# Kernel optimization log

Hardware: AMD Instinct MI355X
Metric: run time of the kernel (lower is better)

## Reference

```python
import jax, jax.numpy as jnp
from jax import lax
import numpy as np

EPS = 4e-3            # geoopt float32 ball boundary eps
MAXNORM = 1.0 - EPS   # c = 1 Poincare ball


def _norm(x):
    return jnp.sqrt(jnp.maximum(jnp.sum(x * x, axis=-1, keepdims=True), 1e-15))


def expmap0(u):
    n = _norm(u)
    return jnp.tanh(n) * u / n


def projx(x):
    n = _norm(x)
    return jnp.where(n > MAXNORM, x * (MAXNORM / n), x)


def mobius_add(x, y):
    x2 = jnp.sum(x * x, -1, keepdims=True)
    y2 = jnp.sum(y * y, -1, keepdims=True)
    xy = jnp.sum(x * y, -1, keepdims=True)
    num = (1.0 + 2.0 * xy + y2) * x + (1.0 - x2) * y
    den = 1.0 + 2.0 * xy + x2 * y2
    return num / jnp.maximum(den, 1e-15)


def mamba_layer(x, inW, convW, convb, xpW, dtW, dtb, A_log, Dp, outW):
    # x: [B,T,H]; inW: [2*Din,H]; convW: [Din,K]; xpW: [R+2N,Din]; dtW: [Din,R]
    B, T, H = x.shape
    Din, N = A_log.shape
    K = convW.shape[-1]
    R = dtW.shape[-1]
    xz = jnp.einsum('bth,dh->btd', x, inW)              # [B,T,2*Din]
    xr, z = jnp.split(xz, 2, axis=-1)
    xc = lax.conv_general_dilated(jnp.transpose(xr, (0, 2, 1)), convW[:, None, :],
                                  (1,), [(K - 1, 0)], feature_group_count=Din)
    u = jax.nn.silu(jnp.transpose(xc + convb[None, :, None], (0, 2, 1)))  # [B,T,Din]
    x_dbl = jnp.einsum('btd,ed->bte', u, xpW)           # [B,T,R+2N]
    dt_r, Bm, Cm = x_dbl[..., :R], x_dbl[..., R:R + N], x_dbl[..., R + N:]
    dt = jax.nn.softplus(jnp.einsum('btr,dr->btd', dt_r, dtW) + dtb)      # [B,T,Din]
    A = -jnp.exp(A_log)                                 # [Din,N]
    dA = jnp.exp(dt[..., None] * A)                     # [B,T,Din,N]
    dBu = dt[..., None] * Bm[:, :, None, :] * u[..., None]

    def step(h, ins):
        dA_t, dBu_t, C_t = ins
        h = dA_t * h + dBu_t                            # [B,Din,N]
        return h, jnp.einsum('bdn,bn->bd', h, C_t)

    h0 = jnp.zeros((B, Din, N), x.dtype)
    _, ys = lax.scan(step, h0, (jnp.moveaxis(dA, 1, 0), jnp.moveaxis(dBu, 1, 0), jnp.moveaxis(Cm, 1, 0)))
    y = jnp.moveaxis(ys, 0, 1) + Dp * u                 # [B,T,Din]
    return jnp.einsum('btd,hd->bth', y * jax.nn.silu(z), outW)


def _encode(xs, inp_W, inp_b, in_proj_W, conv_W, conv_b, xproj_W, dt_W, dt_b, A_log, D_skip, out_W, outp_W, outp_b):
    # xs: [4,B,T,1]; params carry leading branch dim 4, then layer dim 3
    def branch(x, iW, ib, ipW, cW, cb, xpW, dW, db, Al, Dp, oW, opW, opb):
        h = jnp.einsum('bti,hi->bth', x, iW) + ib
        for l in range(ipW.shape[0]):
            h = mamba_layer(h, ipW[l], cW[l], cb[l], xpW[l], dW[l], db[l], Al[l], Dp[l], oW[l])
        return jnp.tanh(jnp.einsum('bth,eh->bte', h, opW) + opb)
    return jax.vmap(branch)(xs, inp_W, inp_b, in_proj_W, conv_W, conv_b, xproj_W, dt_W, dt_b, A_log, D_skip, out_W, outp_W, outp_b)


def setup_inputs() -> dict:
    key = jax.random.key(0)
    ks = jax.random.split(key, 24)
    Br, B, T, H, Din, N, K, R, E, L = 4, 32, 1024, 64, 128, 16, 4, 4, 32, 3

    def rn(k, shape, s=0.05):
        return jax.random.normal(k, shape, jnp.float32) * s

    A_init = jnp.log(jnp.arange(1, N + 1, dtype=jnp.float32))
    return {
        'trend': jax.random.normal(ks[0], (B, T, 1), jnp.float32),
        'seasonal_weekly': jax.random.normal(ks[1], (B, T, 1), jnp.float32),
        'seasonal_daily': jax.random.normal(ks[2], (B, T, 1), jnp.float32),
        'residual': jax.random.normal(ks[3], (B, T, 1), jnp.float32),
        'inp_W': rn(ks[4], (Br, H, 1), 0.5),
        'inp_b': rn(ks[5], (Br, H)),
        'in_proj_W': rn(ks[6], (Br, L, 2 * Din, H)),
        'conv_W': rn(ks[7], (Br, L, Din, K), 0.2),
        'conv_b': rn(ks[8], (Br, L, Din)),
        'xproj_W': rn(ks[9], (Br, L, R + 2 * N, Din)),
        'dt_W': rn(ks[10], (Br, L, Din, R), 0.2),
        'dt_b': rn(ks[11], (Br, L, Din), 0.5) - 4.0,  # softplus(dt_b) small
        'A_log': jnp.tile(A_init, (Br, L, Din, 1)) + rn(ks[12], (Br, L, Din, N), 0.01),
        'D_skip': jnp.ones((Br, L, Din), jnp.float32) + rn(ks[13], (Br, L, Din), 0.01),
        'out_W': rn(ks[14], (Br, L, H, Din)),
        'outp_W': rn(ks[15], (Br, E, H)),
        'outp_b': rn(ks[16], (Br, E)),
    }


def reference(trend, seasonal_weekly, seasonal_daily, residual, inp_W, inp_b, in_proj_W, conv_W, conv_b, xproj_W, dt_W, dt_b, A_log, D_skip, out_W, outp_W, outp_b):
    xs = jnp.stack([trend, seasonal_weekly, seasonal_daily, residual], 0)  # [4,B,T,1]
    z = _encode(xs, inp_W, inp_b, in_proj_W, conv_W, conv_b, xproj_W, dt_W, dt_b, A_log, D_skip, out_W, outp_W, outp_b)  # [4,B,T,E]
    zh = projx(expmap0(z))
    t, w, d, r = zh[0], zh[1], zh[2], zh[3]
    comb = projx(mobius_add(mobius_add(t, mobius_add(w, d)), r))
    # stacked [trend_h, weekly_h, daily_h, residual_h, combined_h]
    return jnp.stack([t, w, d, r, comb], 0)
```

## Files before the change

kernel.cpp:

```cpp
#include <hip/hip_runtime.h>
#include <math.h>

#define TT 1024
#define DIN 128
#define HH 64
#define NN 16
#define EE 32
#define LL 3
#define BB 32

__device__ __forceinline__ float siluf(float x) { return x / (1.f + __expf(-x)); }

typedef __attribute__((ext_vector_type(8))) short bf16x8;
typedef __attribute__((ext_vector_type(4))) float f32x4;

__device__ __forceinline__ void split2(float x, ushort& hi, ushort& lo) {
  unsigned u = __float_as_uint(x);
  hi = (ushort)(u >> 16);
  float rem = x - __uint_as_float((u >> 16) << 16);
  lo = (ushort)(__float_as_uint(rem) >> 16);
}

__global__ __launch_bounds__(256) void k_xz(
    const float* __restrict__ x0, const float* __restrict__ x1,
    const float* __restrict__ x2, const float* __restrict__ x3,
    const float* __restrict__ h, const float* __restrict__ inprojW,
    const float* __restrict__ inpW, const float* __restrict__ inpb,
    float* __restrict__ xr, float* __restrict__ zb, int br0, int l) {
  __shared__ __align__(16) ushort Hh[64][72], Hl[64][72];
  __shared__ __align__(16) ushort Wh[64][72], Wl[64][72];
  const int tid = threadIdx.x;
  const int b  = blockIdx.y;
  const int t0 = blockIdx.x * 64;
  const int br = br0 + (b >> 5);
  const float* Hg = h + ((size_t)b * TT + t0) * HH;
  const int row = tid >> 2, c0 = (tid & 3) * 16;
  {
    float xv = 0.f;
    if (l == 0) {
      int bb = b & 31;
      const float* xp = (br == 0) ? x0 : (br == 1) ? x1 : (br == 2) ? x2 : x3;
      xv = xp[bb * TT + t0 + row];
    }
    #pragma unroll
    for (int q = 0; q < 4; ++q) {
      float4 hv;
      if (l == 0) {
        float4 w4 = *(const float4*)(inpW + br * HH + c0 + q * 4);
        float4 b4 = *(const float4*)(inpb + br * HH + c0 + q * 4);
        hv.x = xv * w4.x + b4.x; hv.y = xv * w4.y + b4.y;
        hv.z = xv * w4.z + b4.z; hv.w = xv * w4.w + b4.w;
      } else {
        hv = *(const float4*)(Hg + (size_t)row * HH + c0 + q * 4);
      }
      ushort h0,h1,h2,h3,l0,l1,l2,l3;
      split2(hv.x,h0,l0); split2(hv.y,h1,l1); split2(hv.z,h2,l2); split2(hv.w,h3,l3);
      *(ushort4*)&Hh[row][c0 + q*4] = make_ushort4(h0,h1,h2,h3);
      *(ushort4*)&Hl[row][c0 + q*4] = make_ushort4(l0,l1,l2,l3);
    }
  }
  const int wave = tid >> 6, lane = tid & 63;
  const int quad = lane >> 4, l16 = lane & 15;
  const int nsub = (wave & 1) * 32, tsub = (wave >> 1) * 32;
  for (int n0 = 0; n0 < 2 * DIN; n0 += 64) {
    const float* Wg = inprojW + (size_t)((br * LL + l) * 2 * DIN + n0) * HH;
    {
      #pragma unroll
      for (int q = 0; q < 4; ++q) {
        float4 wv = *(const float4*)(Wg + (size_t)row * HH + c0 + q * 4);
        ushort h0,h1,h2,h3,l0,l1,l2,l3;
        split2(wv.x,h0,l0); split2(wv.y,h1,l1); split2(wv.z,h2,l2); split2(wv.w,h3,l3);
        *(ushort4*)&Wh[row][c0 + q*4] = make_ushort4(h0,h1,h2,h3);
        *(ushort4*)&Wl[row][c0 + q*4] = make_ushort4(l0,l1,l2,l3);
      }
    }
    __syncthreads();
    f32x4 acc[2][2] = {};
    #pragma unroll
    for (int k0 = 0; k0 < 64; k0 += 32) {
      bf16x8 Ah[2], Al[2], Bh[2], Bl[2];
      #pragma unroll
      for (int i = 0; i < 2; ++i) {
        Ah[i] = *(const bf16x8*)&Wh[nsub + i*16 + l16][k0 + quad*8];
        Al[i] = *(const bf16x8*)&Wl[nsub + i*16 + l16][k0 + quad*8];
        Bh[i] = *(const bf16x8*)&Hh[tsub + i*16 + l16][k0 + quad*8];
        Bl[i] = *(const bf16x8*)&Hl[tsub + i*16 + l16][k0 + quad*8];
      }
      #pragma unroll
      for (int i = 0; i < 2; ++i)
        #pragma unroll
        for (int j = 0; j < 2; ++j) {
          acc[i][j] = __builtin_amdgcn_mfma_f32_16x16x32_bf16(Ah[i], Bh[j], acc[i][j], 0, 0, 0);
          acc[i][j] = __builtin_amdgcn_mfma_f32_16x16x32_bf16(Ah[i], Bl[j], acc[i][j], 0, 0, 0);
          acc[i][j] = __builtin_amdgcn_mfma_f32_16x16x32_bf16(Al[i], Bh[j], acc[i][j], 0, 0, 0);
        }
    }
    #pragma unroll
    for (int i = 0; i < 2; ++i) {
      #pragma unroll
      for (int r = 0; r < 4; ++r) {
        int n = n0 + nsub + i*16 + quad*4 + r;
        float* dst = (n < DIN) ? (xr + ((size_t)b * DIN + n) * TT)
                               : (zb + ((size_t)b * DIN + (n - DIN)) * TT);
        #pragma unroll
        for (int j = 0; j < 2; ++j)
          dst[t0 + tsub + j*16 + l16] = acc[i][j][r];
      }
    }
    __syncthreads();
  }
}

__global__ __launch_bounds__(256) void k_xdbl(
    const float* __restrict__ xr, const float* __restrict__ convW,
    const float* __restrict__ convb, const float* __restrict__ xprojW,
    const float* __restrict__ dtW, const float* __restrict__ dtb,
    float* __restrict__ u, float* __restrict__ dt,
    float* __restrict__ Bm, float* __restrict__ Cm,
    int br0, int l) {
  __shared__ __align__(16) float Xr[16][72];
  __shared__ __align__(16) float As2[32][68];
  __shared__ __align__(16) float Ws2[32][48];
  __shared__ __align__(16) float Xs[40][68];
  const int tid = threadIdx.x;
  const int b  = blockIdx.y;
  const int t0 = blockIdx.x * 64;
  const int br = br0 + (b >> 5);
  const float* W = xprojW + (size_t)((br * LL + l) * 36) * DIN;
  const int rowk = tid >> 4, c4 = tid & 15;
  const int wave = tid >> 6, lane = tid & 63;
  const int quad = lane >> 4, l16 = lane & 15;
  const int tw = wave * 16;
  f32x4 acc[3] = {};
  for (int k0 = 0; k0 < DIN; k0 += 32) {
    #pragma unroll
    for (int ks = 0; ks < 32; ks += 16) {
      __syncthreads();
      {
        const float* src = xr + ((size_t)b * DIN + k0 + ks + rowk) * TT + t0;
        *(float4*)&Xr[rowk][4 + c4 * 4] = *(const float4*)(src + c4 * 4);
        if (tid < 16) {
          float4 hv = make_float4(0.f, 0.f, 0.f, 0.f);
          if (t0 > 0) hv = *(const float4*)(xr + ((size_t)b * DIN + k0 + ks + tid) * TT + t0 - 4);
          *(float4*)&Xr[tid][0] = hv;
        }
      }
      __syncthreads();
      {
        int d = k0 + ks + rowk;
        const float* w = convW + (size_t)((br * LL + l) * DIN + d) * 4;
        float w0 = w[0], w1 = w[1], w2 = w[2], w3 = w[3];
        float cb = convb[(br * LL + l) * DIN + d];
        int i0 = c4 * 4;
        float o[4];
        #pragma unroll
        for (int q = 0; q < 4; ++q) {
          int j = i0 + q;
          float a = Xr[rowk][j+1]*w0 + Xr[rowk][j+2]*w1 + Xr[rowk][j+3]*w2 + Xr[rowk][j+4]*w3 + cb;
          o[q] = siluf(a);
        }
        float4 uo = make_float4(o[0], o[1], o[2], o[3]);
        *(float4*)&As2[ks + rowk][i0] = uo;
        *(float4*)(u + ((size_t)b * DIN + d) * TT + t0 + i0) = uo;
      }
    }
    for (int idx = tid; idx < 1536; idx += 256) {
      int jj = idx >> 5, kk = idx & 31;
      Ws2[kk][jj] = (jj < 36) ? W[(size_t)jj * DIN + k0 + kk] : 0.f;
    }
    __syncthreads();
    ushort bh[8], bl[8];
    #pragma unroll
    for (int j = 0; j < 8; ++j) {
      float v = As2[quad * 8 + j][tw + l16];
      split2(v, bh[j], bl[j]);
    }
    bf16x8 Bh = *(bf16x8*)bh, Bl = *(bf16x8*)bl;
    #pragma unroll
    for (int nf = 0; nf < 3; ++nf) {
      ushort wh[8], wl[8];
      #pragma unroll
      for (int j = 0; j < 8; ++j) {
        float v = Ws2[quad * 8 + j][nf * 16 + l16];
        split2(v, wh[j], wl[j]);
      }
      bf16x8 Wh = *(bf16x8*)wh, Wl = *(bf16x8*)wl;
      acc[nf] = __builtin_amdgcn_mfma_f32_16x16x32_bf16(Wh, Bh, acc[nf], 0, 0, 0);
      acc[nf] = __builtin_amdgcn_mfma_f32_16x16x32_bf16(Wh, Bl, acc[nf], 0, 0, 0);
      acc[nf] = __builtin_amdgcn_mfma_f32_16x16x32_bf16(Wl, Bh, acc[nf], 0, 0, 0);
    }
  }
  __syncthreads();
  #pragma unroll
  for (int nf = 0; nf < 3; ++nf) {
    #pragma unroll
    for (int r = 0; r < 4; ++r) {
      int n = nf * 16 + quad * 4 + r;
      if (n < 40) Xs[n][tw + l16] = acc[nf][r];
    }
  }
  __syncthreads();
  {
    int n = tid >> 4, i0 = (tid & 15) * 4;
    *(float4*)(Bm + ((size_t)b * NN + n) * TT + t0 + i0) = *(float4*)&Xs[4 + n][i0];
    *(float4*)(Cm + ((size_t)b * NN + n) * TT + t0 + i0) = *(float4*)&Xs[20 + n][i0];
  }
  {
    int d = tid >> 1, half = tid & 1;
    const float* wd = dtW + (size_t)((br * LL + l) * DIN + d) * 4;
    float w0 = wd[0], w1 = wd[1], w2 = wd[2], w3 = wd[3];
    float bias = dtb[(br * LL + l) * DIN + d];
    float* dtp = dt + ((size_t)b * DIN + d) * TT + t0 + half * 32;
    #pragma unroll
    for (int g8 = 0; g8 < 8; ++g8) {
      float o[4];
      #pragma unroll
      for (int q = 0; q < 4; ++q) {
        int i = half * 32 + g8 * 4 + q;
        float s = Xs[0][i]*w0 + Xs[1][i]*w1 + Xs[2][i]*w2 + Xs[3][i]*w3 + bias;
        float e = __expf(-fabsf(s));
        o[q] = fmaxf(s, 0.f) + __logf(1.f + e);
      }
      *(float4*)(dtp + g8*4) = make_float4(o[0], o[1], o[2], o[3]);
    }
  }
}

__global__ __launch_bounds__(256) void k_scan1(
    const float* __restrict__ dtc, const float* __restrict__ u,
    const float* __restrict__ Bm, const float* __restrict__ Cm,
    const float* __restrict__ A_log, const float* __restrict__ D_skip,
    float* __restrict__ Hloc, float* __restrict__ g, float* __restrict__ sdt,
    int br0, int l) {
  __shared__ __align__(16) float Bl[16][66];
  __shared__ __align__(16) float Cl[16][66];
  const int bx  = blockIdx.x;
  const int b   = bx >> 5;
  const int rem = bx & 31;
  const int c   = rem >> 1;
  const int dh  = rem & 1;
  const int tid = threadIdx.x;
  {
    int row = tid >> 4, cc = (tid & 15) * 4;
    float4 bv = *(const float4*)(Bm + ((size_t)b * NN + row) * TT + c * 64 + cc);
    *(float2*)&Bl[row][cc]     = make_float2(bv.x, bv.y);
    *(float2*)&Bl[row][cc + 2] = make_float2(bv.z, bv.w);
    float4 cv = *(const float4*)(Cm + ((size_t)b * NN + row) * TT + c * 64 + cc);
    *(float2*)&Cl[row][cc]     = make_float2(cv.x, cv.y);
    *(float2*)&Cl[row][cc + 2] = make_float2(cv.z, cv.w);
  }
  __syncthreads();
  const int d  = dh * 64 + (tid >> 2);
  const int n0 = (tid & 3) * 4;
  const int br = br0 + (b >> 5);
  const int wbase = (br * LL + l) * DIN + d;
  float Ac[4];
  #pragma unroll
  for (int j = 0; j < 4; ++j) Ac[j] = -__expf(A_log[(size_t)wbase * NN + n0 + j]);
  float Dp = D_skip[wbase];
  const float* dtp = dtc + ((size_t)b * DIN + d) * TT + c * 64;
  const float* up = u + ((size_t)b * DIN + d) * TT + c * 64;
  float* gp = g + ((size_t)b * DIN + d) * TT + c * 64;
  float hst[4] = {0.f, 0.f, 0.f, 0.f};
  float sd = 0.f;
  for (int t0 = 0; t0 < 64; t0 += 8) {
    float4 dq0 = *(const float4*)(dtp + t0);
    float4 dq1 = *(const float4*)(dtp + t0 + 4);
    float4 uq0 = *(const float4*)(up + t0);
    float4 uq1 = *(const float4*)(up + t0 + 4);
    float dts[8] = {dq0.x, dq0.y, dq0.z, dq0.w, dq1.x, dq1.y, dq1.z, dq1.w};
    float us[8]  = {uq0.x, uq0.y, uq0.z, uq0.w, uq1.x, uq1.y, uq1.z, uq1.w};
    float Bs[4][8], Cr[4][8];
    #pragma unroll
    for (int j = 0; j < 4; ++j) {
      float2 b0 = *(const float2*)&Bl[n0 + j][t0];
      float2 b1 = *(const float2*)&Bl[n0 + j][t0 + 2];
      float2 b2 = *(const float2*)&Bl[n0 + j][t0 + 4];
      float2 b3 = *(const float2*)&Bl[n0 + j][t0 + 6];
      Bs[j][0]=b0.x; Bs[j][1]=b0.y; Bs[j][2]=b1.x; Bs[j][3]=b1.y;
      Bs[j][4]=b2.x; Bs[j][5]=b2.y; Bs[j][6]=b3.x; Bs[j][7]=b3.y;
      float2 c0 = *(const float2*)&Cl[n0 + j][t0];
      float2 c1 = *(const float2*)&Cl[n0 + j][t0 + 2];
      float2 c2 = *(const float2*)&Cl[n0 + j][t0 + 4];
      float2 c3 = *(const float2*)&Cl[n0 + j][t0 + 6];
      Cr[j][0]=c0.x; Cr[j][1]=c0.y; Cr[j][2]=c1.x; Cr[j][3]=c1.y;
      Cr[j][4]=c2.x; Cr[j][5]=c2.y; Cr[j][6]=c3.x; Cr[j][7]=c3.y;
    }
    float yo[8];
    #pragma unroll
    for (int s = 0; s < 8; ++s) {
      float dtv = dts[s], uv = us[s];
      sd += dtv;
      float du = dtv * uv;
      float acc = 0.f;
      #pragma unroll
      for (int j = 0; j < 4; ++j) {
        float dA = __expf(dtv * Ac[j]);
        hst[j] = dA * hst[j] + du * Bs[j][s];
        acc += hst[j] * Cr[j][s];
      }
      acc += __shfl_xor(acc, 1, 4);
      acc += __shfl_xor(acc, 2, 4);
      yo[s] = acc + Dp * uv;
    }
    if ((tid & 3) == 0) {
      *(float4*)(gp + t0)     = make_float4(yo[0], yo[1], yo[2], yo[3]);
      *(float4*)(gp + t0 + 4) = make_float4(yo[4], yo[5], yo[6], yo[7]);
    }
  }
  *(float4*)(Hloc + (((size_t)b * DIN + d) * 16 + c) * 16 + n0) =
      make_float4(hst[0], hst[1], hst[2], hst[3]);
  if ((tid & 3) == 0) sdt[((size_t)b * DIN + d) * 16 + c] = sd;
}

__global__ __launch_bounds__(256) void k_scan2(
    const float* __restrict__ dtc, const float* __restrict__ Cm,
    const float* __restrict__ A_log, const float* __restrict__ Hloc,
    const float* __restrict__ sdt, float* __restrict__ g, int br0, int l) {
  __shared__ __align__(16) float Cl[16][68];
  __shared__ __align__(16) float Dl[32][68];
  __shared__ __align__(16) float HinL[32][16];
  const int bx  = blockIdx.x;
  const int b   = bx / 60;
  const int rem = bx % 60;
  const int c   = (rem >> 2) + 1;
  const int dq  = rem & 3;
  const int tid = threadIdx.x;
  const int br  = br0 + (b >> 5);
  {
    int row = tid >> 4, cc = (tid & 15) * 4;
    *(float4*)&Cl[row][cc] = *(const float4*)(Cm + ((size_t)b * NN + row) * TT + c * 64 + cc);
  }
  const int dloc = tid >> 3, tg = tid & 7;
  const int d  = dq * 32 + dloc;
  {
    const float* dp = dtc + ((size_t)b * DIN + d) * TT + c * 64 + tg * 8;
    *(float4*)&Dl[dloc][tg * 8]     = *(const float4*)dp;
    *(float4*)&Dl[dloc][tg * 8 + 4] = *(const float4*)(dp + 4);
  }
  {
    int n0 = (tid & 7) * 2;
    int wbase = (br * LL + l) * DIN + d;
    float a0 = -__expf(A_log[(size_t)wbase * NN + n0]);
    float a1 = -__expf(A_log[(size_t)wbase * NN + n0 + 1]);
    float h0 = 0.f, h1 = 0.f;
    const float* sp  = sdt + ((size_t)b * DIN + d) * 16;
    const float* hlb = Hloc + ((size_t)b * DIN + d) * 256;
    for (int cc = 0; cc < c; ++cc) {
      float sdv = sp[cc];
      float2 hl = *(const float2*)(hlb + cc * 16 + n0);
      h0 = __expf(a0 * sdv) * h0 + hl.x;
      h1 = __expf(a1 * sdv) * h1 + hl.y;
    }
    HinL[dloc][n0] = h0;
    HinL[dloc][n0 + 1] = h1;
  }
  __syncthreads();
  float cd8[8];
  {
    float run = 0.f;
    for (int t = 0; t < tg * 8; ++t) run += Dl[dloc][t];
    #pragma unroll
    for (int s = 0; s < 8; ++s) { run += Dl[dloc][tg * 8 + s]; cd8[s] = run; }
  }
  const float* al = A_log + (size_t)((br * LL + l) * DIN + d) * NN;
  float Ac16[16];
  #pragma unroll
  for (int n = 0; n < 16; ++n) Ac16[n] = -__expf(al[n]);
  size_t off = ((size_t)b * DIN + d) * TT + c * 64 + tg * 8;
  float* gp = g + off;
  float4 y0 = *(float4*)gp;
  float4 y1 = *(float4*)(gp + 4);
  float y8[8] = {y0.x, y0.y, y0.z, y0.w, y1.x, y1.y, y1.z, y1.w};
  const int tbase = tg * 8;
  #pragma unroll
  for (int n = 0; n < 16; ++n) {
    float hv = HinL[dloc][n];
    float an = Ac16[n];
    #pragma unroll
    for (int s = 0; s < 8; ++s)
      y8[s] += Cl[n][tbase + s] * __expf(an * cd8[s]) * hv;
  }
  *(float4*)gp       = make_float4(y8[0], y8[1], y8[2], y8[3]);
  *(float4*)(gp + 4) = make_float4(y8[4], y8[5], y8[6], y8[7]);
}

__global__ __launch_bounds__(256) void k_out(
    const float* __restrict__ graw, const float* __restrict__ zb,
    const float* __restrict__ outW, float* __restrict__ h, int br0, int l) {
  __shared__ __align__(16) ushort Ah_[64][72], Al_[64][72];
  __shared__ __align__(16) ushort Bh_[64][72], Bl_[64][72];
  const int tid = threadIdx.x;
  const int b  = blockIdx.y;
  const int t0 = blockIdx.x * 64;
  const int br = br0 + (b >> 5);
  const float* Wg = outW + (size_t)((br * LL + l) * HH) * DIN;
  const int wave = tid >> 6, lane = tid & 63;
  const int quad = lane >> 4, l16 = lane & 15;
  const int hsub = (wave & 1) * 32, tsub = (wave >> 1) * 32;
  f32x4 acc[2][2] = {};
  for (int k0 = 0; k0 < DIN; k0 += 64) {
    __syncthreads();
    {
      int row = tid >> 2, c0 = (tid & 3) * 16;
      #pragma unroll
      for (int q = 0; q < 4; ++q) {
        float4 wv = *(const float4*)(Wg + (size_t)row * DIN + k0 + c0 + q * 4);
        ushort h0,h1,h2,h3,l0,l1,l2,l3;
        split2(wv.x,h0,l0); split2(wv.y,h1,l1); split2(wv.z,h2,l2); split2(wv.w,h3,l3);
        *(ushort4*)&Ah_[row][c0 + q*4] = make_ushort4(h0,h1,h2,h3);
        *(ushort4*)&Al_[row][c0 + q*4] = make_ushort4(l0,l1,l2,l3);
        size_t off = ((size_t)b * DIN + k0 + row) * TT + t0 + c0 + q * 4;
        float4 gv = *(const float4*)(graw + off);
        float4 zv = *(const float4*)(zb + off);
        float a0 = gv.x * siluf(zv.x), a1 = gv.y * siluf(zv.y);
        float a2 = gv.z * siluf(zv.z), a3 = gv.w * siluf(zv.w);
        split2(a0,h0,l0); split2(a1,h1,l1); split2(a2,h2,l2); split2(a3,h3,l3);
        *(ushort4*)&Bh_[row][c0 + q*4] = make_ushort4(h0,h1,h2,h3);
        *(ushort4*)&Bl_[row][c0 + q*4] = make_ushort4(l0,l1,l2,l3);
      }
    }
    __syncthreads();
    #pragma unroll
    for (int kk = 0; kk < 64; kk += 32) {
      bf16x8 Ahf[2], Alf[2], Bhf[2], Blf[2];
      #pragma unroll
      for (int i = 0; i < 2; ++i) {
        Ahf[i] = *(const bf16x8*)&Ah_[hsub + i*16 + l16][kk + quad*8];
        Alf[i] = *(const bf16x8*)&Al_[hsub + i*16 + l16][kk + quad*8];
        Bhf[i] = *(const bf16x8*)&Bh_[tsub + i*16 + l16][kk + quad*8];
        Blf[i] = *(const bf16x8*)&Bl_[tsub + i*16 + l16][kk + quad*8];
      }
      #pragma unroll
      for (int i = 0; i < 2; ++i)
        #pragma unroll
        for (int j = 0; j < 2; ++j) {
          acc[i][j] = __builtin_amdgcn_mfma_f32_16x16x32_bf16(Ahf[i], Bhf[j], acc[i][j], 0, 0, 0);
          acc[i][j] = __builtin_amdgcn_mfma_f32_16x16x32_bf16(Ahf[i], Blf[j], acc[i][j], 0, 0, 0);
          acc[i][j] = __builtin_amdgcn_mfma_f32_16x16x32_bf16(Alf[i], Bhf[j], acc[i][j], 0, 0, 0);
        }
    }
  }
  #pragma unroll
  for (int i = 0; i < 2; ++i) {
    int hh0 = hsub + i*16 + quad*4;
    #pragma unroll
    for (int j = 0; j < 2; ++j) {
      int t = t0 + tsub + j*16 + l16;
      *(f32x4*)(h + ((size_t)b * TT + t) * HH + hh0) = acc[i][j];
    }
  }
}

__global__ __launch_bounds__(256) void k_ze(
    const float* __restrict__ h, const float* __restrict__ outpW,
    const float* __restrict__ outpb, float* __restrict__ ze, int br0) {
  __shared__ __align__(16) float As[16][132];
  __shared__ __align__(16) float Ws[16][36];
  __shared__ __align__(16) float Cs[128][36];
  const int tid = threadIdx.x;
  const int b  = blockIdx.y;
  const int t0 = blockIdx.x * 128;
  const int br = br0 + (b >> 5);
  const float* W = outpW + (size_t)br * EE * HH;
  float acc[4][4] = {};
  const int ti = tid & 31, ni = tid >> 5;
  for (int k0 = 0; k0 < HH; k0 += 16) {
    __syncthreads();
    {
      int i = tid >> 1, kq = (tid & 1) * 8;
      const float* src = h + ((size_t)b * TT + t0 + i) * HH + k0 + kq;
      float4 a0 = *(const float4*)src;
      float4 a1 = *(const float4*)(src + 4);
      As[kq+0][i]=a0.x; As[kq+1][i]=a0.y; As[kq+2][i]=a0.z; As[kq+3][i]=a0.w;
      As[kq+4][i]=a1.x; As[kq+5][i]=a1.y; As[kq+6][i]=a1.z; As[kq+7][i]=a1.w;
    }
    for (int idx = tid; idx < 512; idx += 256) {
      int jj = idx >> 4, kk = idx & 15;
      Ws[kk][jj] = W[(size_t)jj * HH + k0 + kk];
    }
    __syncthreads();
    #pragma unroll
    for (int kk = 0; kk < 16; ++kk) {
      float4 a = *(const float4*)&As[kk][ti * 4];
      float4 w = *(const float4*)&Ws[kk][ni * 4];
      acc[0][0] += a.x*w.x; acc[0][1] += a.x*w.y; acc[0][2] += a.x*w.z; acc[0][3] += a.x*w.w;
      acc[1][0] += a.y*w.x; acc[1][1] += a.y*w.y; acc[1][2] += a.y*w.z; acc[1][3] += a.y*w.w;
      acc[2][0] += a.z*w.x; acc[2][1] += a.z*w.y; acc[2][2] += a.z*w.z; acc[2][3] += a.z*w.w;
      acc[3][0] += a.w*w.x; acc[3][1] += a.w*w.y; acc[3][2] += a.w*w.z; acc[3][3] += a.w*w.w;
    }
  }
  __syncthreads();
  float bj[4];
  #pragma unroll
  for (int c = 0; c < 4; ++c) bj[c] = outpb[br * EE + ni*4 + c];
  #pragma unroll
  for (int r = 0; r < 4; ++r)
    #pragma unroll
    for (int c = 0; c < 4; ++c)
      Cs[ti*4+r][ni*4+c] = tanhf(acc[r][c] + bj[c]);
  __syncthreads();
  int i = tid >> 1, j16 = (tid & 1) * 16;
  float* dst = ze + (((size_t)(br0 * 32 + b)) * TT + t0 + i) * EE + j16;
  #pragma unroll
  for (int q = 0; q < 4; ++q)
    *(float4*)(dst + q*4) = *(float4*)&Cs[i][j16 + q*4];
}

__device__ __forceinline__ void mobius_add32(const float* x, const float* y, float* o) {
  float x2 = 0.f, y2 = 0.f, xy = 0.f;
  #pragma unroll
  for (int i = 0; i < 32; ++i) { x2 += x[i]*x[i]; y2 += y[i]*y[i]; xy += x[i]*y[i]; }
  float ca  = 1.f + 2.f*xy + y2;
  float cb  = 1.f - x2;
  float den = 1.f + 2.f*xy + x2*y2;
  float inv = 1.f / fmaxf(den, 1e-15f);
  #pragma unroll
  for (int i = 0; i < 32; ++i) o[i] = (ca*x[i] + cb*y[i]) * inv;
}

__global__ __launch_bounds__(256) void k_hyper(const float* __restrict__ ze,
                                               float* __restrict__ out) {
  int idx = blockIdx.x * 256 + threadIdx.x;
  int b = idx >> 10, t = idx & 1023;
  float v[4][32];
  #pragma unroll
  for (int br = 0; br < 4; ++br) {
    const float* p = ze + (((size_t)br * BB + b) * TT + t) * EE;
    float s = 0.f;
    #pragma unroll
    for (int e = 0; e < 32; ++e) { v[br][e] = p[e]; s += v[br][e]*v[br][e]; }
    float nr = sqrtf(fmaxf(s, 1e-15f));
    float sc = tanhf(nr) / nr;
    float s2 = 0.f;
    #pragma unroll
    for (int e = 0; e < 32; ++e) { v[br][e] *= sc; s2 += v[br][e]*v[br][e]; }
    float n2 = sqrtf(fmaxf(s2, 1e-15f));
    if (n2 > 0.996f) {
      float sc2 = 0.996f / n2;
      #pragma unroll
      for (int e = 0; e < 32; ++e) v[br][e] *= sc2;
    }
    float* o = out + (((size_t)br * BB + b) * TT + t) * EE;
    #pragma unroll
    for (int e = 0; e < 32; ++e) o[e] = v[br][e];
  }
  float m1[32], m2[32];
  mobius_add32(v[1], v[2], m1);
  mobius_add32(v[0], m1, m2);
  mobius_add32(m2, v[3], m1);
  float s = 0.f;
  #pragma unroll
  for (int e = 0; e < 32; ++e) s += m1[e]*m1[e];
  float n = sqrtf(fmaxf(s, 1e-15f));
  if (n > 0.996f) {
    float sc = 0.996f / n;
    #pragma unroll
    for (int e = 0; e < 32; ++e) m1[e] *= sc;
  }
  float* o = out + (((size_t)4 * BB + b) * TT + t) * EE;
  #pragma unroll
  for (int e = 0; e < 32; ++e) o[e] = m1[e];
}

extern "C" void kernel_launch(void* const* d_in, const int* in_sizes, int n_in,
                              void* d_out, int out_size, void* d_ws, size_t ws_size,
                              hipStream_t stream) {
  const float* xs0 = (const float*)d_in[0];
  const float* xs1 = (const float*)d_in[1];
  const float* xs2 = (const float*)d_in[2];
  const float* xs3 = (const float*)d_in[3];
  const float* inpW   = (const float*)d_in[4];
  const float* inpb   = (const float*)d_in[5];
  const float* iprojW = (const float*)d_in[6];
  const float* convW  = (const float*)d_in[7];
  const float* convb  = (const float*)d_in[8];
  const float* xprojW = (const float*)d_in[9];
  const float* dtW    = (const float*)d_in[10];
  const float* dtb    = (const float*)d_in[11];
  const float* A_log  = (const float*)d_in[12];
  const float* D_skip = (const float*)d_in[13];
  const float* outW   = (const float*)d_in[14];
  const float* outpW  = (const float*)d_in[15];
  const float* outpb  = (const float*)d_in[16];
  float* out = (float*)d_out;
  float* ws  = (float*)d_ws;

  const size_t zeF = (size_t)4 * BB * TT * EE;
  const size_t perBl = 65536 + 4 * 131072 + 2 * 16384 + 2048;
  auto needBytes = [&](int NB) { return (zeF + (size_t)NB * 32 * perBl) * 4; };
  int NB = 4;
  if (needBytes(4) > ws_size) NB = 2;
  if (NB == 2 && needBytes(2) > ws_size) NB = 1;
  const int nbl = NB * 32;

  float* ze = ws;
  float* h  = ze + zeF;
  float* xr = h  + (size_t)nbl * 65536;
  float* zb = xr + (size_t)nbl * 131072;
  float* u  = zb + (size_t)nbl * 131072;
  float* dt = u  + (size_t)nbl * 131072;
  float* Bm = dt + (size_t)nbl * 131072;
  float* Cm = Bm + (size_t)nbl * 16384;
  float* sdt = Cm + (size_t)nbl * 16384;
  float* g  = xr;
  float* Hloc = h;

  for (int br0 = 0; br0 < 4; br0 += NB) {
    for (int l = 0; l < LL; ++l) {
      k_xz   <<<dim3(16, nbl), 256, 0, stream>>>(xs0, xs1, xs2, xs3, h, iprojW,
                                                 inpW, inpb, xr, zb, br0, l);
      k_xdbl <<<dim3(16, nbl), 256, 0, stream>>>(xr, convW, convb, xprojW, dtW, dtb,
                                                 u, dt, Bm, Cm, br0, l);
      k_scan1<<<nbl * 32, 256, 0, stream>>>(dt, u, Bm, Cm, A_log, D_skip,
                                            Hloc, g, sdt, br0, l);
      k_scan2<<<nbl * 60, 256, 0, stream>>>(dt, Cm, A_log, Hloc, sdt, g, br0, l);
      k_out  <<<dim3(16, nbl), 256, 0, stream>>>(g, zb, outW, h, br0, l);
    }
    k_ze<<<dim3(8, nbl), 256, 0, stream>>>(h, outpW, outpb, ze, br0);
  }
  k_hyper<<<BB * TT / 256, 256, 0, stream>>>(ze, out);
}
```

Measured before the change: 1.018 ms.

## Presplit weights to bf16 hi/lo once and read fragments from global

Adds a one-time kernel that splits the in_proj, x_proj and out_proj weights into bf16 hi/lo arrays in the workspace. The GEMM kernels then load MFMA weight fragments straight from global memory instead of converting and staging them in LDS on every block, which also removes some shared memory and barriers. scan1 now writes the running cumulative dt back into the dt buffer, so scan2 no longer needs its serial prefix-sum loop. scan1 also prefetches the next chunk's dt/u values, and the conv step uses vectorised LDS reads. The cost is uncoalesced-ish global fragment loads and extra workspace.

```diff
diff --git a/kernel.cpp b/kernel.cpp
--- a/kernel.cpp
+++ b/kernel.cpp
@@ -21,21 +21,51 @@
   lo = (ushort)(__float_as_uint(rem) >> 16);
 }
 
+#define WXZ_N 196608
+#define WXD_N 73728
+#define WOUT_N 98304
+
+__global__ __launch_bounds__(256) void k_presplit(
+    const float* __restrict__ iprojW, const float* __restrict__ xprojW,
+    const float* __restrict__ outW,
+    ushort* __restrict__ WxzH, ushort* __restrict__ WxzL,
+    ushort* __restrict__ WxdH, ushort* __restrict__ WxdL,
+    ushort* __restrict__ WoH, ushort* __restrict__ WoL) {
+  int idx = blockIdx.x * 256 + threadIdx.x;
+  if (idx < WXZ_N) {
+    ushort h, l;
+    split2(iprojW[idx], h, l);
+    WxzH[idx] = h; WxzL[idx] = l;
+  }
+  if (idx < WXD_N) {
+    int k = idx & 127, r = (idx >> 7) % 48, bl = idx / (48 * 128);
+    float v = (r < 36) ? xprojW[((size_t)(bl * 36 + r)) * 128 + k] : 0.f;
+    ushort h, l;
+    split2(v, h, l);
+    WxdH[idx] = h; WxdL[idx] = l;
+  }
+  if (idx < WOUT_N) {
+    ushort h, l;
+    split2(outW[idx], h, l);
+    WoH[idx] = h; WoL[idx] = l;
+  }
+}
+
 __global__ __launch_bounds__(256) void k_xz(
     const float* __restrict__ x0, const float* __restrict__ x1,
     const float* __restrict__ x2, const float* __restrict__ x3,
-    const float* __restrict__ h, const float* __restrict__ inprojW,
+    const float* __restrict__ h, const ushort* __restrict__ WH,
+    const ushort* __restrict__ WL,
     const float* __restrict__ inpW, const float* __restrict__ inpb,
     float* __restrict__ xr, float* __restrict__ zb, int br0, int l) {
   __shared__ __align__(16) ushort Hh[64][72], Hl[64][72];
-  __shared__ __align__(16) ushort Wh[64][72], Wl[64][72];
   const int tid = threadIdx.x;
   const int b  = blockIdx.y;
   const int t0 = blockIdx.x * 64;
   const int br = br0 + (b >> 5);
   const float* Hg = h + ((size_t)b * TT + t0) * HH;
-  const int row = tid >> 2, c0 = (tid & 3) * 16;
   {
+    const int row = tid >> 2, c0 = (tid & 3) * 16;
     float xv = 0.f;
     if (l == 0) {
       int bb = b & 31;
@@ -59,30 +89,21 @@
       *(ushort4*)&Hl[row][c0 + q*4] = make_ushort4(l0,l1,l2,l3);
     }
   }
+  __syncthreads();
   const int wave = tid >> 6, lane = tid & 63;
   const int quad = lane >> 4, l16 = lane & 15;
   const int nsub = (wave & 1) * 32, tsub = (wave >> 1) * 32;
+  const size_t wbase = (size_t)(br * LL + l) * 256;
   for (int n0 = 0; n0 < 2 * DIN; n0 += 64) {
-    const float* Wg = inprojW + (size_t)((br * LL + l) * 2 * DIN + n0) * HH;
-    {
-      #pragma unroll
-      for (int q = 0; q < 4; ++q) {
-        float4 wv = *(const float4*)(Wg + (size_t)row * HH + c0 + q * 4);
-        ushort h0,h1,h2,h3,l0,l1,l2,l3;
-        split2(wv.x,h0,l0); split2(wv.y,h1,l1); split2(wv.z,h2,l2); split2(wv.w,h3,l3);
-        *(ushort4*)&Wh[row][c0 + q*4] = make_ushort4(h0,h1,h2,h3);
-        *(ushort4*)&Wl[row][c0 + q*4] = make_ushort4(l0,l1,l2,l3);
-      }
-    }
-    __syncthreads();
     f32x4 acc[2][2] = {};
     #pragma unroll
     for (int k0 = 0; k0 < 64; k0 += 32) {
       bf16x8 Ah[2], Al[2], Bh[2], Bl[2];
       #pragma unroll
       for (int i = 0; i < 2; ++i) {
-        Ah[i] = *(const bf16x8*)&Wh[nsub + i*16 + l16][k0 + quad*8];
-        Al[i] = *(const bf16x8*)&Wl[nsub + i*16 + l16][k0 + quad*8];
+        size_t ro = (wbase + n0 + nsub + i * 16 + l16) * 64 + k0 + quad * 8;
+        Ah[i] = *(const bf16x8*)(WH + ro);
+        Al[i] = *(const bf16x8*)(WL + ro);
         Bh[i] = *(const bf16x8*)&Hh[tsub + i*16 + l16][k0 + quad*8];
         Bl[i] = *(const bf16x8*)&Hl[tsub + i*16 + l16][k0 + quad*8];
       }
@@ -107,30 +128,29 @@
           dst[t0 + tsub + j*16 + l16] = acc[i][j][r];
       }
     }
-    __syncthreads();
   }
 }
 
 __global__ __launch_bounds__(256) void k_xdbl(
     const float* __restrict__ xr, const float* __restrict__ convW,
-    const float* __restrict__ convb, const float* __restrict__ xprojW,
-    const float* __restrict__ dtW, const float* __restrict__ dtb,
+    const float* __restrict__ convb, const ushort* __restrict__ WH,
+    const ushort* __restrict__ WL, const float* __restrict__ dtW,
+    const float* __restrict__ dtb,
     float* __restrict__ u, float* __restrict__ dt,
     float* __restrict__ Bm, float* __restrict__ Cm,
     int br0, int l) {
   __shared__ __align__(16) float Xr[16][72];
-  __shared__ __align__(16) float As2[32][68];
-  __shared__ __align__(16) float Ws2[32][48];
+  __shared__ __align__(16) float As2[32][65];
   __shared__ __align__(16) float Xs[40][68];
   const int tid = threadIdx.x;
   const int b  = blockIdx.y;
   const int t0 = blockIdx.x * 64;
   const int br = br0 + (b >> 5);
-  const float* W = xprojW + (size_t)((br * LL + l) * 36) * DIN;
   const int rowk = tid >> 4, c4 = tid & 15;
   const int wave = tid >> 6, lane = tid & 63;
   const int quad = lane >> 4, l16 = lane & 15;
   const int tw = wave * 16;
+  const size_t wb48 = (size_t)(br * LL + l) * 48 * 128;
   f32x4 acc[3] = {};
   for (int k0 = 0; k0 < DIN; k0 += 32) {
     #pragma unroll
@@ -151,43 +171,35 @@
         const float* w = convW + (size_t)((br * LL + l) * DIN + d) * 4;
         float w0 = w[0], w1 = w[1], w2 = w[2], w3 = w[3];
         float cb = convb[(br * LL + l) * DIN + d];
-        int i0 = c4 * 4;
-        float o[4];
-        #pragma unroll
-        for (int q = 0; q < 4; ++q) {
-          int j = i0 + q;
-          float a = Xr[rowk][j+1]*w0 + Xr[rowk][j+2]*w1 + Xr[rowk][j+3]*w2 + Xr[rowk][j+4]*w3 + cb;
-          o[q] = siluf(a);
-        }
-        float4 uo = make_float4(o[0], o[1], o[2], o[3]);
-        *(float4*)&As2[ks + rowk][i0] = uo;
-        *(float4*)(u + ((size_t)b * DIN + d) * TT + t0 + i0) = uo;
-      }
-    }
-    for (int idx = tid; idx < 1536; idx += 256) {
-      int jj = idx >> 5, kk = idx & 31;
-      Ws2[kk][jj] = (jj < 36) ? W[(size_t)jj * DIN + k0 + kk] : 0.f;
+        int ic = c4 * 4;
+        float4 Av = *(const float4*)&Xr[rowk][ic];
+        float4 Bv = *(const float4*)&Xr[rowk][ic + 4];
+        float o0 = siluf(Av.y*w0 + Av.z*w1 + Av.w*w2 + Bv.x*w3 + cb);
+        float o1 = siluf(Av.z*w0 + Av.w*w1 + Bv.x*w2 + Bv.y*w3 + cb);
+        float o2 = siluf(Av.w*w0 + Bv.x*w1 + Bv.y*w2 + Bv.z*w3 + cb);
+        float o3 = siluf(Bv.x*w0 + Bv.y*w1 + Bv.z*w2 + Bv.w*w3 + cb);
+        *(float4*)(u + ((size_t)b * DIN + d) * TT + t0 + ic) = make_float4(o0, o1, o2, o3);
+        As2[ks + rowk][ic]     = o0;
+        As2[ks + rowk][ic + 1] = o1;
+        As2[ks + rowk][ic + 2] = o2;
+        As2[ks + rowk][ic + 3] = o3;
+      }
     }
     __syncthreads();
     ushort bh[8], bl[8];
     #pragma unroll
     for (int j = 0; j < 8; ++j) {
-      float v = As2[quad * 8 + j][tw + l16];
-      split2(v, bh[j], bl[j]);
+      split2(As2[quad * 8 + j][tw + l16], bh[j], bl[j]);
     }
     bf16x8 Bh = *(bf16x8*)bh, Bl = *(bf16x8*)bl;
     #pragma unroll
     for (int nf = 0; nf < 3; ++nf) {
-      ushort wh[8], wl[8];
-      #pragma unroll
-      for (int j = 0; j < 8; ++j) {
-        float v = Ws2[quad * 8 + j][nf * 16 + l16];
-        split2(v, wh[j], wl[j]);
-      }
-      bf16x8 Wh = *(bf16x8*)wh, Wl = *(bf16x8*)wl;
-      acc[nf] = __builtin_amdgcn_mfma_f32_16x16x32_bf16(Wh, Bh, acc[nf], 0, 0, 0);
-      acc[nf] = __builtin_amdgcn_mfma_f32_16x16x32_bf16(Wh, Bl, acc[nf], 0, 0, 0);
-      acc[nf] = __builtin_amdgcn_mfma_f32_16x16x32_bf16(Wl, Bh, acc[nf], 0, 0, 0);
+      size_t ro = wb48 + (size_t)(nf * 16 + l16) * 128 + k0 + quad * 8;
+      bf16x8 Whf = *(const bf16x8*)(WH + ro);
+      bf16x8 Wlf = *(const bf16x8*)(WL + ro);
+      acc[nf] = __builtin_amdgcn_mfma_f32_16x16x32_bf16(Whf, Bh, acc[nf], 0, 0, 0);
+      acc[nf] = __builtin_amdgcn_mfma_f32_16x16x32_bf16(Whf, Bl, acc[nf], 0, 0, 0);
+      acc[nf] = __builtin_amdgcn_mfma_f32_16x16x32_bf16(Wlf, Bh, acc[nf], 0, 0, 0);
     }
   }
   __syncthreads();
@@ -227,7 +239,7 @@
 }
 
 __global__ __launch_bounds__(256) void k_scan1(
-    const float* __restrict__ dtc, const float* __restrict__ u,
+    float* __restrict__ dtc, const float* __restrict__ u,
     const float* __restrict__ Bm, const float* __restrict__ Cm,
     const float* __restrict__ A_log, const float* __restrict__ D_skip,
     float* __restrict__ Hloc, float* __restrict__ g, float* __restrict__ sdt,
@@ -258,18 +270,26 @@
   #pragma unroll
   for (int j = 0; j < 4; ++j) Ac[j] = -__expf(A_log[(size_t)wbase * NN + n0 + j]);
   float Dp = D_skip[wbase];
-  const float* dtp = dtc + ((size_t)b * DIN + d) * TT + c * 64;
+  float* dtp = dtc + ((size_t)b * DIN + d) * TT + c * 64;
   const float* up = u + ((size_t)b * DIN + d) * TT + c * 64;
   float* gp = g + ((size_t)b * DIN + d) * TT + c * 64;
   float hst[4] = {0.f, 0.f, 0.f, 0.f};
   float sd = 0.f;
+  float4 d0 = *(const float4*)(dtp);
+  float4 d1 = *(const float4*)(dtp + 4);
+  float4 u0 = *(const float4*)(up);
+  float4 u1 = *(const float4*)(up + 4);
+  #pragma unroll
   for (int t0 = 0; t0 < 64; t0 += 8) {
-    float4 dq0 = *(const float4*)(dtp + t0);
-    float4 dq1 = *(const float4*)(dtp + t0 + 4);
-    float4 uq0 = *(const float4*)(up + t0);
-    float4 uq1 = *(const float4*)(up + t0 + 4);
-    float dts[8] = {dq0.x, dq0.y, dq0.z, dq0.w, dq1.x, dq1.y, dq1.z, dq1.w};
-    float us[8]  = {uq0.x, uq0.y, uq0.z, uq0.w, uq1.x, uq1.y, uq1.z, uq1.w};
+    float4 nd0, nd1, nu0, nu1;
+    if (t0 < 56) {
+      nd0 = *(const float4*)(dtp + t0 + 8);
+      nd1 = *(const float4*)(dtp + t0 + 12);
+      nu0 = *(const float4*)(up + t0 + 8);
+      nu1 = *(const float4*)(up + t0 + 12);
+    }
+    float dts[8] = {d0.x, d0.y, d0.z, d0.w, d1.x, d1.y, d1.z, d1.w};
+    float us[8]  = {u0.x, u0.y, u0.z, u0.w, u1.x, u1.y, u1.z, u1.w};
     float Bs[4][8], Cr[4][8];
     #pragma unroll
     for (int j = 0; j < 4; ++j) {
@@ -286,11 +306,12 @@
       Cr[j][0]=c0.x; Cr[j][1]=c0.y; Cr[j][2]=c1.x; Cr[j][3]=c1.y;
       Cr[j][4]=c2.x; Cr[j][5]=c2.y; Cr[j][6]=c3.x; Cr[j][7]=c3.y;
     }
-    float yo[8];
+    float yo[8], cds[8];
     #pragma unroll
     for (int s = 0; s < 8; ++s) {
       float dtv = dts[s], uv = us[s];
       sd += dtv;
+      cds[s] = sd;
       float du = dtv * uv;
       float acc = 0.f;
       #pragma unroll
@@ -306,7 +327,10 @@
     if ((tid & 3) == 0) {
       *(float4*)(gp + t0)     = make_float4(yo[0], yo[1], yo[2], yo[3]);
       *(float4*)(gp + t0 + 4) = make_float4(yo[4], yo[5], yo[6], yo[7]);
-    }
+      *(float4*)(dtp + t0)     = make_float4(cds[0], cds[1], cds[2], cds[3]);
+      *(float4*)(dtp + t0 + 4) = make_float4(cds[4], cds[5], cds[6], cds[7]);
+    }
+    d0 = nd0; d1 = nd1; u0 = nu0; u1 = nu1;
   }
   *(float4*)(Hloc + (((size_t)b * DIN + d) * 16 + c) * 16 + n0) =
       make_float4(hst[0], hst[1], hst[2], hst[3]);
@@ -314,11 +338,10 @@
 }
 
 __global__ __launch_bounds__(256) void k_scan2(
-    const float* __restrict__ dtc, const float* __restrict__ Cm,
+    const float* __restrict__ cdc, const float* __restrict__ Cm,
     const float* __restrict__ A_log, const float* __restrict__ Hloc,
     const float* __restrict__ sdt, float* __restrict__ g, int br0, int l) {
   __shared__ __align__(16) float Cl[16][68];
-  __shared__ __align__(16) float Dl[32][68];
   __shared__ __align__(16) float HinL[32][16];
   const int bx  = blockIdx.x;
   const int b   = bx / 60;
@@ -333,11 +356,12 @@
   }
   const int dloc = tid >> 3, tg = tid & 7;
   const int d  = dq * 32 + dloc;
-  {
-    const float* dp = dtc + ((size_t)b * DIN + d) * TT + c * 64 + tg * 8;
-    *(float4*)&Dl[dloc][tg * 8]     = *(const float4*)dp;
-    *(float4*)&Dl[dloc][tg * 8 + 4] = *(const float4*)(dp + 4);
-  }
+  size_t off = ((size_t)b * DIN + d) * TT + c * 64 + tg * 8;
+  float* gp = g + off;
+  float4 y0 = *(const float4*)gp;
+  float4 y1 = *(const float4*)(gp + 4);
+  float4 cq0 = *(const float4*)(cdc + off);
+  float4 cq1 = *(const float4*)(cdc + off + 4);
   {
     int n0 = (tid & 7) * 2;
     int wbase = (br * LL + l) * DIN + d;
@@ -356,21 +380,11 @@
     HinL[dloc][n0 + 1] = h1;
   }
   __syncthreads();
-  float cd8[8];
-  {
-    float run = 0.f;
-    for (int t = 0; t < tg * 8; ++t) run += Dl[dloc][t];
-    #pragma unroll
-    for (int s = 0; s < 8; ++s) { run += Dl[dloc][tg * 8 + s]; cd8[s] = run; }
-  }
+  float cd8[8] = {cq0.x, cq0.y, cq0.z, cq0.w, cq1.x, cq1.y, cq1.z, cq1.w};
   const float* al = A_log + (size_t)((br * LL + l) * DIN + d) * NN;
   float Ac16[16];
   #pragma unroll
   for (int n = 0; n < 16; ++n) Ac16[n] = -__expf(al[n]);
-  size_t off = ((size_t)b * DIN + d) * TT + c * 64 + tg * 8;
-  float* gp = g + off;
-  float4 y0 = *(float4*)gp;
-  float4 y1 = *(float4*)(gp + 4);
   float y8[8] = {y0.x, y0.y, y0.z, y0.w, y1.x, y1.y, y1.z, y1.w};
   const int tbase = tg * 8;
   #pragma unroll
@@ -387,17 +401,17 @@
 
 __global__ __launch_bounds__(256) void k_out(
     const float* __restrict__ graw, const float* __restrict__ zb,
-    const float* __restrict__ outW, float* __restrict__ h, int br0, int l) {
-  __shared__ __align__(16) ushort Ah_[64][72], Al_[64][72];
+    const ushort* __restrict__ WH, const ushort* __restrict__ WL,
+    float* __restrict__ h, int br0, int l) {
   __shared__ __align__(16) ushort Bh_[64][72], Bl_[64][72];
   const int tid = threadIdx.x;
   const int b  = blockIdx.y;
   const int t0 = blockIdx.x * 64;
   const int br = br0 + (b >> 5);
-  const float* Wg = outW + (size_t)((br * LL + l) * HH) * DIN;
   const int wave = tid >> 6, lane = tid & 63;
   const int quad = lane >> 4, l16 = lane & 15;
   const int hsub = (wave & 1) * 32, tsub = (wave >> 1) * 32;
+  const size_t wb = (size_t)(br * LL + l) * 64;
   f32x4 acc[2][2] = {};
   for (int k0 = 0; k0 < DIN; k0 += 64) {
     __syncthreads();
@@ -405,16 +419,12 @@
       int row = tid >> 2, c0 = (tid & 3) * 16;
       #pragma unroll
       for (int q = 0; q < 4; ++q) {
-        float4 wv = *(const float4*)(Wg + (size_t)row * DIN + k0 + c0 + q * 4);
-        ushort h0,h1,h2,h3,l0,l1,l2,l3;
-        split2(wv.x,h0,l0); split2(wv.y,h1,l1); split2(wv.z,h2,l2); split2(wv.w,h3,l3);
-        *(ushort4*)&Ah_[row][c0 + q*4] = make_ushort4(h0,h1,h2,h3);
-        *(ushort4*)&Al_[row][c0 + q*4] = make_ushort4(l0,l1,l2,l3);
         size_t off = ((size_t)b * DIN + k0 + row) * TT + t0 + c0 + q * 4;
         float4 gv = *(const float4*)(graw + off);
         float4 zv = *(const float4*)(zb + off);
         float a0 = gv.x * siluf(zv.x), a1 = gv.y * siluf(zv.y);
         float a2 = gv.z * siluf(zv.z), a3 = gv.w * siluf(zv.w);
+        ushort h0,h1,h2,h3,l0,l1,l2,l3;
         split2(a0,h0,l0); split2(a1,h1,l1); split2(a2,h2,l2); split2(a3,h3,l3);
         *(ushort4*)&Bh_[row][c0 + q*4] = make_ushort4(h0,h1,h2,h3);
         *(ushort4*)&Bl_[row][c0 + q*4] = make_ushort4(l0,l1,l2,l3);
@@ -426,8 +436,9 @@
       bf16x8 Ahf[2], Alf[2], Bhf[2], Blf[2];
       #pragma unroll
       for (int i = 0; i < 2; ++i) {
-        Ahf[i] = *(const bf16x8*)&Ah_[hsub + i*16 + l16][kk + quad*8];
-        Alf[i] = *(const bf16x8*)&Al_[hsub + i*16 + l16][kk + quad*8];
+        size_t ro = (wb + hsub + i * 16 + l16) * 128 + k0 + kk + quad * 8;
+        Ahf[i] = *(const bf16x8*)(WH + ro);
+        Alf[i] = *(const bf16x8*)(WL + ro);
         Bhf[i] = *(const bf16x8*)&Bh_[tsub + i*16 + l16][kk + quad*8];
         Blf[i] = *(const bf16x8*)&Bl_[tsub + i*16 + l16][kk + quad*8];
       }
@@ -584,11 +595,21 @@
   const float* outpW  = (const float*)d_in[15];
   const float* outpb  = (const float*)d_in[16];
   float* out = (float*)d_out;
-  float* ws  = (float*)d_ws;
+
+  const size_t wUshorts = 2 * (WXZ_N + WXD_N + WOUT_N);
+  ushort* WxzH = (ushort*)d_ws;
+  ushort* WxzL = WxzH + WXZ_N;
+  ushort* WxdH = WxzL + WXZ_N;
+  ushort* WxdL = WxdH + WXD_N;
+  ushort* WoH  = WxdL + WXD_N;
+  ushort* WoL  = WoH + WOUT_N;
+  float* ws = (float*)(WoL + WOUT_N);
 
   const size_t zeF = (size_t)4 * BB * TT * EE;
   const size_t perBl = 65536 + 4 * 131072 + 2 * 16384 + 2048;
-  auto needBytes = [&](int NB) { return (zeF + (size_t)NB * 32 * perBl) * 4; };
+  auto needBytes = [&](int NB) {
+    return (zeF + (size_t)NB * 32 * perBl) * 4 + wUshorts * 2;
+  };
   int NB = 4;
   if (needBytes(4) > ws_size) NB = 2;
   if (NB == 2 && needBytes(2) > ws_size) NB = 1;
@@ -606,16 +627,19 @@
   float* g  = xr;
   float* Hloc = h;
 
+  k_presplit<<<WXZ_N / 256, 256, 0, stream>>>(iprojW, xprojW, outW,
+                                              WxzH, WxzL, WxdH, WxdL, WoH, WoL);
+
   for (int br0 = 0; br0 < 4; br0 += NB) {
     for (int l = 0; l < LL; ++l) {
-      k_xz   <<<dim3(16, nbl), 256, 0, stream>>>(xs0, xs1, xs2, xs3, h, iprojW,
-                                                 inpW, inpb, xr, zb, br0, l);
-      k_xdbl <<<dim3(16, nbl), 256, 0, stream>>>(xr, convW, convb, xprojW, dtW, dtb,
-                                                 u, dt, Bm, Cm, br0, l);
+      k_xz   <<<dim3(16, nbl), 256, 0, stream>>>(xs0, xs1, xs2, xs3, h,
+                                                 WxzH, WxzL, inpW, inpb, xr, zb, br0, l);
+      k_xdbl <<<dim3(16, nbl), 256, 0, stream>>>(xr, convW, convb, WxdH, WxdL,
+                                                 dtW, dtb, u, dt, Bm, Cm, br0, l);
       k_scan1<<<nbl * 32, 256, 0, stream>>>(dt, u, Bm, Cm, A_log, D_skip,
                                             Hloc, g, sdt, br0, l);
       k_scan2<<<nbl * 60, 256, 0, stream>>>(dt, Cm, A_log, Hloc, sdt, g, br0, l);
-      k_out  <<<dim3(16, nbl), 256, 0, stream>>>(g, zb, outW, h, br0, l);
+      k_out  <<<dim3(16, nbl), 256, 0, stream>>>(g, zb, WoH, WoL, h, br0, l);
     }
     k_ze<<<dim3(8, nbl), 256, 0, stream>>>(h, outpW, outpb, ze, br0);
   }
```

Measured after the change: 1.092 ms. 1.07x slower.
